# Optimization experiments

Measured on AMD Instinct MI355X. Metric: run time of the kernel, lower is better.

The kernel has to match this reference:

```python
import jax, jax.numpy as jnp
import numpy as np

B, N, DIN, DH, DOUT = 4096, 16, 256, 256, 256  # batch rows, num_variables, per-var dims


def _ln(x, g, b, eps=1e-5):
    m = jnp.mean(x, axis=-1, keepdims=True)
    v = jnp.var(x, axis=-1, keepdims=True)
    return (x - m) * jax.lax.rsqrt(v + eps) * g + b


def setup_inputs() -> dict:
    key = jax.random.key(0)
    ks = jax.random.split(key, 10)
    s = 0.02
    f32 = jnp.float32
    return {
        "x": jax.random.normal(ks[0], (B, N, DIN), f32),
        # per-variable GRN params, stacked along variable axis (batched GEMMs)
        "vW2": s * jax.random.normal(ks[1], (N, DIN, DH), f32),
        "vb2": jnp.zeros((N, DH), f32),
        "vW1": s * jax.random.normal(ks[2], (N, DH, DOUT), f32),
        "vb1": jnp.zeros((N, DOUT), f32),
        "vW4": s * jax.random.normal(ks[3], (N, DOUT, DOUT), f32),
        "vb4": jnp.zeros((N, DOUT), f32),
        "vW5": s * jax.random.normal(ks[4], (N, DOUT, DOUT), f32),
        "vb5": jnp.zeros((N, DOUT), f32),
        "vlng": jnp.ones((N, DOUT), f32),
        "vlnb": jnp.zeros((N, DOUT), f32),
        # concat GRN params (operate on flattened n*in features)
        "cW2": s * jax.random.normal(ks[5], (N * DIN, N * DH), f32),
        "cb2": jnp.zeros((N * DH,), f32),
        "cW1": s * jax.random.normal(ks[6], (N * DH, N * DOUT), f32),
        "cb1": jnp.zeros((N * DOUT,), f32),
        "cW4": s * jax.random.normal(ks[7], (N * DOUT, N * DOUT), f32),
        "cb4": jnp.zeros((N * DOUT,), f32),
        "cW5": s * jax.random.normal(ks[8], (N * DOUT, N * DOUT), f32),
        "cb5": jnp.zeros((N * DOUT,), f32),
        "clng": jnp.ones((N * DOUT,), f32),
        "clnb": jnp.zeros((N * DOUT,), f32),
    }


def reference(x, vW2, vb2, vW1, vb1, vW4, vb4, vW5, vb5, vlng, vlnb,
              cW2, cb2, cW1, cb1, cW4, cb4, cW5, cb5, clng, clnb):
    b = x.shape[0]
    flat = x.reshape(b, N * DIN)                       # torch.cat(inputs) over feature dim
    # ---- concat GRN: ELU dense -> dense -> GLU -> residual layernorm ----
    h = jax.nn.elu(flat @ cW2 + cb2)                   # [b, N*DH]
    e1 = h @ cW1 + cb1                                 # [b, N*DOUT]
    g = jax.nn.sigmoid(e1 @ cW4 + cb4) * (e1 @ cW5 + cb5)
    c = _ln(flat + g, clng, clnb)                      # [b, N*DOUT] (in==out, identity skip)
    # ---- softmax selection weights over the variable axis ----
    w = jax.nn.softmax(c.reshape(b, N, DOUT), axis=1)  # [b, N, DOUT]
    # ---- per-variable GRNs as batched GEMMs over the variable axis ----
    hv = jax.nn.elu(jnp.einsum('bni,nih->bnh', x, vW2) + vb2)
    e1v = jnp.einsum('bnh,nho->bno', hv, vW1) + vb1
    gv = (jax.nn.sigmoid(jnp.einsum('bno,nop->bnp', e1v, vW4) + vb4)
          * (jnp.einsum('bno,nop->bnp', e1v, vW5) + vb5))
    yv = _ln(x + gv, vlng, vlnb)                       # [b, N, DOUT]
    # ---- weighted combine (v^T @ x in the original) ----
    return jnp.sum(w * yv, axis=1)                     # [b, DOUT]
```

## Files before the change

### kernel.cpp

```cpp
#include <hip/hip_runtime.h>
#include <hip/hip_bf16.h>
#include <math.h>

typedef __hip_bfloat16 bf16;
typedef __attribute__((ext_vector_type(8))) short short8;
typedef __attribute__((ext_vector_type(4))) float f32x4;

#define DEV __device__ __forceinline__

DEV void gload_lds16(const bf16* g, bf16* l) {
    __builtin_amdgcn_global_load_lds(
        (__attribute__((address_space(1))) void*)(g),
        (__attribute__((address_space(3))) void*)(l), 16, 0, 0);
}

template<int ACT, bool DUAL>
__global__ __launch_bounds__(256, 2)
void gemm_k(const bf16* __restrict__ A, int lda, long aBatch,
            const bf16* __restrict__ B1p, const bf16* __restrict__ B2p,
            int ldb, long bBatch,
            const float* __restrict__ bias1p, const float* __restrict__ bias2p,
            long biasBatch,
            bf16* __restrict__ C, int ldc, long cBatch, int K)
{
    const int bz = blockIdx.z;
    A   += (long)bz * aBatch;
    const bf16* B1 = B1p + (long)bz * bBatch;
    const float* bias1 = bias1p + (long)bz * biasBatch;
    C   += (long)bz * cBatch;
    const bf16* B2 = nullptr;
    const float* bias2 = nullptr;
    if constexpr (DUAL) {
        B2 = B2p + (long)bz * bBatch;
        bias2 = bias2p + (long)bz * biasBatch;
    }

    const int rowBase = blockIdx.y * 128;
    const int colBase = blockIdx.x * 128;

    __shared__ bf16 As[128 * 32];
    __shared__ bf16 Bs[128 * 32];
    __shared__ bf16 Bs2[DUAL ? 128 * 32 : 8];

    const int tid  = threadIdx.x;
    const int wid  = tid >> 6;
    const int lane = tid & 63;
    const int wr = wid >> 1, wc = wid & 1;
    const int lr = lane & 15, lg = lane >> 4;

    f32x4 acc[4][4] = {};
    f32x4 acc2[4][4] = {};

    const int e0 = wid * 512 + lane * 8;
    const int sr = e0 >> 5;
    const int sc = e0 & 31;

    const bf16* a0 = A  + (long)(rowBase + sr)      * lda + sc;
    const bf16* a1 = A  + (long)(rowBase + sr + 64) * lda + sc;
    const bf16* b0 = B1 + (long)(colBase + sr)      * ldb + sc;
    const bf16* b1 = B1 + (long)(colBase + sr + 64) * ldb + sc;
    const bf16* d0 = nullptr; const bf16* d1 = nullptr;
    if constexpr (DUAL) {
        d0 = B2 + (long)(colBase + sr)      * ldb + sc;
        d1 = B2 + (long)(colBase + sr + 64) * ldb + sc;
    }

    bf16* AsW = As + wid * 512;
    bf16* BsW = Bs + wid * 512;
    bf16* Bs2W = nullptr;
    if constexpr (DUAL) Bs2W = Bs2 + wid * 512;

    for (int k0 = 0; k0 < K; k0 += 32) {
        gload_lds16(a0 + k0, AsW);
        gload_lds16(a1 + k0, AsW + 2048);
        gload_lds16(b0 + k0, BsW);
        gload_lds16(b1 + k0, BsW + 2048);
        if constexpr (DUAL) {
            gload_lds16(d0 + k0, Bs2W);
            gload_lds16(d1 + k0, Bs2W + 2048);
        }
        __syncthreads();

        short8 a[4], bb[4], b2[4];
        #pragma unroll
        for (int m = 0; m < 4; m++)
            a[m] = *(const short8*)(As + (wr * 64 + m * 16 + lr) * 32 + lg * 8);
        #pragma unroll
        for (int n = 0; n < 4; n++)
            bb[n] = *(const short8*)(Bs + (wc * 64 + n * 16 + lr) * 32 + lg * 8);
        if constexpr (DUAL) {
            #pragma unroll
            for (int n = 0; n < 4; n++)
                b2[n] = *(const short8*)(Bs2 + (wc * 64 + n * 16 + lr) * 32 + lg * 8);
        }

        #pragma unroll
        for (int m = 0; m < 4; m++) {
            #pragma unroll
            for (int n = 0; n < 4; n++) {
                acc[m][n] = __builtin_amdgcn_mfma_f32_16x16x32_bf16(a[m], bb[n], acc[m][n], 0, 0, 0);
                if constexpr (DUAL)
                    acc2[m][n] = __builtin_amdgcn_mfma_f32_16x16x32_bf16(a[m], b2[n], acc2[m][n], 0, 0, 0);
            }
        }
        __syncthreads();
    }

    #pragma unroll
    for (int m = 0; m < 4; m++) {
        const int row = rowBase + wr * 64 + m * 16 + lg * 4;
        #pragma unroll
        for (int n = 0; n < 4; n++) {
            const int col = colBase + wc * 64 + n * 16 + lr;
            const float bv1 = bias1[col];
            float bv2 = 0.f;
            if constexpr (DUAL) bv2 = bias2[col];
            #pragma unroll
            for (int i = 0; i < 4; i++) {
                float v = acc[m][n][i] + bv1;
                if constexpr (ACT == 1) v = v > 0.f ? v : expm1f(v);
                if constexpr (DUAL) {
                    float v2 = acc2[m][n][i] + bv2;
                    v = v2 / (1.f + expf(-v));
                }
                C[(long)(row + i) * ldc + col] = __float2bfloat16(v);
            }
        }
    }
}

__global__ __launch_bounds__(256)
void cvt_k(const float* __restrict__ in, bf16* __restrict__ out)
{
    const long i = ((long)blockIdx.x * 256 + threadIdx.x) * 8;
    float4 u = *(const float4*)(in + i);
    float4 v = *(const float4*)(in + i + 4);
    bf16 t[8];
    t[0] = __float2bfloat16(u.x); t[1] = __float2bfloat16(u.y);
    t[2] = __float2bfloat16(u.z); t[3] = __float2bfloat16(u.w);
    t[4] = __float2bfloat16(v.x); t[5] = __float2bfloat16(v.y);
    t[6] = __float2bfloat16(v.z); t[7] = __float2bfloat16(v.w);
    *(short8*)(out + i) = *(short8*)t;
}

struct TPtrs { const float* s[4]; bf16* d[4]; };

__global__ __launch_bounds__(256)
void transpose_cvt_k(TPtrs p, int R, int nsub)
{
    const int z = blockIdx.z;
    const int widx = z / nsub, sub = z - widx * nsub;
    const float* __restrict__ in = p.s[widx] + (long)sub * R * R;
    bf16* __restrict__ outp = p.d[widx] + (long)sub * R * R;

    __shared__ float tile[32][33];
    const int c0 = blockIdx.x * 32, r0 = blockIdx.y * 32;
    const int tx = threadIdx.x & 31, ty = threadIdx.x >> 5;
    #pragma unroll
    for (int i = 0; i < 4; i++)
        tile[ty + i * 8][tx] = in[(long)(r0 + ty + i * 8) * R + c0 + tx];
    __syncthreads();
    #pragma unroll
    for (int i = 0; i < 4; i++)
        outp[(long)(c0 + ty + i * 8) * R + r0 + tx] = __float2bfloat16(tile[tx][ty + i * 8]);
}

DEV float2 block_reduce2_bcast(float a, float b, float* lds)
{
    const int lane = threadIdx.x & 63, wid = threadIdx.x >> 6;
    #pragma unroll
    for (int off = 32; off > 0; off >>= 1) {
        a += __shfl_down(a, off, 64);
        b += __shfl_down(b, off, 64);
    }
    __syncthreads();
    if (lane == 0) { lds[wid] = a; lds[wid + 4] = b; }
    __syncthreads();
    float2 r;
    r.x = lds[0] + lds[1] + lds[2] + lds[3];
    r.y = lds[4] + lds[5] + lds[6] + lds[7];
    return r;
}

__global__ __launch_bounds__(256)
void ln_softmax_k(const float* __restrict__ x, const bf16* __restrict__ g,
                  const float* __restrict__ gamma, const float* __restrict__ beta,
                  bf16* __restrict__ w)
{
    const int b = blockIdx.x, d = threadIdx.x;
    const long base = (long)b * 4096;
    __shared__ float red[8];

    float s[16];
    float sum = 0.f, sumsq = 0.f;
    #pragma unroll
    for (int n = 0; n < 16; n++) {
        float v = x[base + n * 256 + d] + __bfloat162float(g[base + n * 256 + d]);
        s[n] = v; sum += v; sumsq += v * v;
    }
    float2 t = block_reduce2_bcast(sum, sumsq, red);
    const float mean = t.x * (1.f / 4096.f);
    const float var  = t.y * (1.f / 4096.f) - mean * mean;
    const float rstd = rsqrtf(var + 1e-5f);

    float mx = -1e30f;
    #pragma unroll
    for (int n = 0; n < 16; n++) {
        float c = (s[n] - mean) * rstd * gamma[n * 256 + d] + beta[n * 256 + d];
        s[n] = c; mx = fmaxf(mx, c);
    }
    float denom = 0.f;
    #pragma unroll
    for (int n = 0; n < 16; n++) { float e = expf(s[n] - mx); s[n] = e; denom += e; }
    const float rden = 1.f / denom;
    #pragma unroll
    for (int n = 0; n < 16; n++)
        w[base + n * 256 + d] = __float2bfloat16(s[n] * rden);
}

__global__ __launch_bounds__(256)
void combine_k(const float* __restrict__ x, const bf16* __restrict__ gv,
               const bf16* __restrict__ w,
               const float* __restrict__ vlng, const float* __restrict__ vlnb,
               float* __restrict__ out)
{
    const int b = blockIdx.x, d = threadIdx.x;
    const long base = (long)b * 4096;
    __shared__ float red[8];
    float acc = 0.f;
    for (int n = 0; n < 16; n++) {
        float v = x[base + n * 256 + d] + __bfloat162float(gv[base + n * 256 + d]);
        float2 t = block_reduce2_bcast(v, v * v, red);
        const float mean = t.x * (1.f / 256.f);
        const float var  = t.y * (1.f / 256.f) - mean * mean;
        const float yv = (v - mean) * rsqrtf(var + 1e-5f) * vlng[n * 256 + d] + vlnb[n * 256 + d];
        acc += __bfloat162float(w[base + n * 256 + d]) * yv;
    }
    out[(long)b * 256 + d] = acc;
}

extern "C" void kernel_launch(void* const* d_in, const int* in_sizes, int n_in,
                              void* d_out, int out_size, void* d_ws, size_t ws_size,
                              hipStream_t stream)
{
    const float* x    = (const float*)d_in[0];
    const float* vW2  = (const float*)d_in[1];
    const float* vb2  = (const float*)d_in[2];
    const float* vW1  = (const float*)d_in[3];
    const float* vb1  = (const float*)d_in[4];
    const float* vW4  = (const float*)d_in[5];
    const float* vb4  = (const float*)d_in[6];
    const float* vW5  = (const float*)d_in[7];
    const float* vb5  = (const float*)d_in[8];
    const float* vlng = (const float*)d_in[9];
    const float* vlnb = (const float*)d_in[10];
    const float* cW2  = (const float*)d_in[11];
    const float* cb2  = (const float*)d_in[12];
    const float* cW1  = (const float*)d_in[13];
    const float* cb1  = (const float*)d_in[14];
    const float* cW4  = (const float*)d_in[15];
    const float* cb4  = (const float*)d_in[16];
    const float* cW5  = (const float*)d_in[17];
    const float* cb5  = (const float*)d_in[18];
    const float* clng = (const float*)d_in[19];
    const float* clnb = (const float*)d_in[20];
    float* out = (float*)d_out;
    (void)n_in; (void)out_size; (void)ws_size;

    const int NB = in_sizes[0] / 4096;
    const long XF = (long)NB * 4096;

    char* ws = (char*)d_ws;
    size_t off = 0;
    auto alloc = [&](size_t bytes) {
        char* p = ws + off;
        off += (bytes + 255) & ~(size_t)255;
        return p;
    };
    bf16* xb   = (bf16*)alloc(XF * 2);
    bf16* cW2t = (bf16*)alloc(4096L * 4096 * 2);
    bf16* cW1t = (bf16*)alloc(4096L * 4096 * 2);
    bf16* cW4t = (bf16*)alloc(4096L * 4096 * 2);
    bf16* cW5t = (bf16*)alloc(4096L * 4096 * 2);
    bf16* vW2t = (bf16*)alloc(16L * 256 * 256 * 2);
    bf16* vW1t = (bf16*)alloc(16L * 256 * 256 * 2);
    bf16* vW4t = (bf16*)alloc(16L * 256 * 256 * 2);
    bf16* vW5t = (bf16*)alloc(16L * 256 * 256 * 2);
    bf16* bufA = (bf16*)alloc(XF * 2);
    bf16* bufB = (bf16*)alloc(XF * 2);
    bf16* bufW = (bf16*)alloc(XF * 2);

    const int MB = NB / 128;

    cvt_k<<<dim3((unsigned)(XF / 2048)), 256, 0, stream>>>(x, xb);

    TPtrs pb;
    pb.s[0] = cW2; pb.s[1] = cW1; pb.s[2] = cW4; pb.s[3] = cW5;
    pb.d[0] = cW2t; pb.d[1] = cW1t; pb.d[2] = cW4t; pb.d[3] = cW5t;
    transpose_cvt_k<<<dim3(128, 128, 4), 256, 0, stream>>>(pb, 4096, 1);

    TPtrs pv;
    pv.s[0] = vW2; pv.s[1] = vW1; pv.s[2] = vW4; pv.s[3] = vW5;
    pv.d[0] = vW2t; pv.d[1] = vW1t; pv.d[2] = vW4t; pv.d[3] = vW5t;
    transpose_cvt_k<<<dim3(8, 8, 64), 256, 0, stream>>>(pv, 256, 16);

    gemm_k<1, false><<<dim3(32, MB, 1), 256, 0, stream>>>(
        xb, 4096, 0, cW2t, nullptr, 4096, 0, cb2, nullptr, 0, bufA, 4096, 0, 4096);
    gemm_k<0, false><<<dim3(32, MB, 1), 256, 0, stream>>>(
        bufA, 4096, 0, cW1t, nullptr, 4096, 0, cb1, nullptr, 0, bufB, 4096, 0, 4096);
    gemm_k<0, true><<<dim3(32, MB, 1), 256, 0, stream>>>(
        bufB, 4096, 0, cW4t, cW5t, 4096, 0, cb4, cb5, 0, bufA, 4096, 0, 4096);
    ln_softmax_k<<<dim3(NB), 256, 0, stream>>>(x, bufA, clng, clnb, bufW);

    gemm_k<1, false><<<dim3(2, MB, 16), 256, 0, stream>>>(
        xb, 4096, 256, vW2t, nullptr, 256, 65536, vb2, nullptr, 256, bufB, 4096, 256, 256);
    gemm_k<0, false><<<dim3(2, MB, 16), 256, 0, stream>>>(
        bufB, 4096, 256, vW1t, nullptr, 256, 65536, vb1, nullptr, 256, bufA, 4096, 256, 256);
    gemm_k<0, true><<<dim3(2, MB, 16), 256, 0, stream>>>(
        bufA, 4096, 256, vW4t, vW5t, 256, 65536, vb4, vb5, 256, bufB, 4096, 256, 256);

    combine_k<<<dim3(NB), 256, 0, stream>>>(x, bufB, bufW, vlng, vlnb, out);
}
```

Before: 1.119 ms.

## Replace GEMM with 256x256 double-buffered pipelined kernel and split GLU GEMMs

Replaces the 128x128 single-buffered GEMM with a 512-thread 256x256 tile kernel. It uses 128KB of dynamic LDS double buffering, swizzled LDS layout, explicit vmcnt waits, quadrant-interleaved MFMA scheduling with setprio, and XCD-aware block remapping. The dual GLU GEMM is split into two single-output GEMMs, and the sigmoid gating moves into the LN/softmax and combine kernels. Dead transposed-weight buffers are reused as scratch for the extra outputs. The aim is better operand reuse and load/compute overlap, at the cost of extra intermediate traffic, fewer blocks per launch (only 16 per batched small GEMM), and more LDS pressure.

```diff
diff --git a/kernel.cpp b/kernel.cpp
--- a/kernel.cpp
+++ b/kernel.cpp
@@ -1,6 +1,7 @@
 #include <hip/hip_runtime.h>
 #include <hip/hip_bf16.h>
 #include <math.h>
+#include <type_traits>
 
 typedef __hip_bfloat16 bf16;
 typedef __attribute__((ext_vector_type(8))) short short8;
@@ -8,125 +9,164 @@
 
 #define DEV __device__ __forceinline__
 
+template<int V> using IC = std::integral_constant<int, V>;
+
 DEV void gload_lds16(const bf16* g, bf16* l) {
     __builtin_amdgcn_global_load_lds(
-        (__attribute__((address_space(1))) void*)(g),
+        (const __attribute__((address_space(1))) void*)(g),
         (__attribute__((address_space(3))) void*)(l), 16, 0, 0);
 }
 
-template<int ACT, bool DUAL>
-__global__ __launch_bounds__(256, 2)
-void gemm_k(const bf16* __restrict__ A, int lda, long aBatch,
-            const bf16* __restrict__ B1p, const bf16* __restrict__ B2p,
-            int ldb, long bBatch,
-            const float* __restrict__ bias1p, const float* __restrict__ bias2p,
-            long biasBatch,
-            bf16* __restrict__ C, int ldc, long cBatch, int K)
-{
+#define VMW(n) do { asm volatile("s_waitcnt vmcnt(" #n ")" ::: "memory"); \
+                    __builtin_amdgcn_sched_barrier(0); } while (0)
+
+template<int ACT>
+__global__ __launch_bounds__(512, 2)
+void gemm256_k(const bf16* __restrict__ Am, int lda, long aBatch,
+               const bf16* __restrict__ Bm, int ldb, long bBatch,
+               const float* __restrict__ biasp, long biasBatch,
+               bf16* __restrict__ Cm, int ldc, long cBatch, int K)
+{
+    extern __shared__ char lds[];
     const int bz = blockIdx.z;
-    A   += (long)bz * aBatch;
-    const bf16* B1 = B1p + (long)bz * bBatch;
-    const float* bias1 = bias1p + (long)bz * biasBatch;
-    C   += (long)bz * cBatch;
-    const bf16* B2 = nullptr;
-    const float* bias2 = nullptr;
-    if constexpr (DUAL) {
-        B2 = B2p + (long)bz * bBatch;
-        bias2 = bias2p + (long)bz * biasBatch;
-    }
-
-    const int rowBase = blockIdx.y * 128;
-    const int colBase = blockIdx.x * 128;
-
-    __shared__ bf16 As[128 * 32];
-    __shared__ bf16 Bs[128 * 32];
-    __shared__ bf16 Bs2[DUAL ? 128 * 32 : 8];
-
-    const int tid  = threadIdx.x;
-    const int wid  = tid >> 6;
-    const int lane = tid & 63;
-    const int wr = wid >> 1, wc = wid & 1;
+    const bf16* A = Am + (long)bz * aBatch;
+    const bf16* B = Bm + (long)bz * bBatch;
+    const float* bias = biasp + (long)bz * biasBatch;
+    bf16* C = Cm + (long)bz * cBatch;
+
+    const int nwg = gridDim.x * gridDim.y;
+    int flat = blockIdx.y * gridDim.x + blockIdx.x;
+    if ((nwg & 7) == 0 && nwg >= 8) flat = (flat & 7) * (nwg >> 3) + (flat >> 3);
+    const int bx = flat % gridDim.x, by = flat / gridDim.x;
+    const int rowBase = by * 256, colBase = bx * 256;
+
+    const int tid = threadIdx.x;
+    const int wid = tid >> 6, lane = tid & 63;
+    const int wr = wid >> 2, wc = wid & 3;
     const int lr = lane & 15, lg = lane >> 4;
 
-    f32x4 acc[4][4] = {};
-    f32x4 acc2[4][4] = {};
-
-    const int e0 = wid * 512 + lane * 8;
-    const int sr = e0 >> 5;
-    const int sc = e0 & 31;
-
-    const bf16* a0 = A  + (long)(rowBase + sr)      * lda + sc;
-    const bf16* a1 = A  + (long)(rowBase + sr + 64) * lda + sc;
-    const bf16* b0 = B1 + (long)(colBase + sr)      * ldb + sc;
-    const bf16* b1 = B1 + (long)(colBase + sr + 64) * ldb + sc;
-    const bf16* d0 = nullptr; const bf16* d1 = nullptr;
-    if constexpr (DUAL) {
-        d0 = B2 + (long)(colBase + sr)      * ldb + sc;
-        d1 = B2 + (long)(colBase + sr + 64) * ldb + sc;
-    }
-
-    bf16* AsW = As + wid * 512;
-    bf16* BsW = Bs + wid * 512;
-    bf16* Bs2W = nullptr;
-    if constexpr (DUAL) Bs2W = Bs2 + wid * 512;
-
-    for (int k0 = 0; k0 < K; k0 += 32) {
-        gload_lds16(a0 + k0, AsW);
-        gload_lds16(a1 + k0, AsW + 2048);
-        gload_lds16(b0 + k0, BsW);
-        gload_lds16(b1 + k0, BsW + 2048);
-        if constexpr (DUAL) {
-            gload_lds16(d0 + k0, Bs2W);
-            gload_lds16(d1 + k0, Bs2W + 2048);
-        }
-        __syncthreads();
-
-        short8 a[4], bb[4], b2[4];
+    const int r     = (tid >> 2) & 15;
+    const int cbyte = (tid & 3) * 16;
+    const int c0    = ((r & 8) ? (cbyte ^ 32) : cbyte) >> 1;
+    const int srow  = (wid >> 1) * 16 + r;
+    const int scol  = (wid & 1) * 32 + c0;
+
+    const bf16* Ap = A + (long)(rowBase + srow) * lda + scol;
+    const bf16* Bp = B + (long)(colBase + srow) * ldb + scol;
+
+    const int cb  = (lr & 8) ? ((lg * 16) ^ 32) : (lg * 16);
+    const int aRd = wr * 8192 + lr * 64 + cb;
+    const int bRd = wc * 4096 + lr * 64 + cb;
+
+    f32x4  acc[2][2][4][2] = {};
+    short8 aF[2][4][2];
+    short8 bF[2][2][2];
+
+    const int T = K >> 6;
+
+    auto stageA = [&](int tt, int h) {
+        bf16* d = (bf16*)(lds + (tt & 1) * 32768 + h * 16384 + wid * 1024);
+        const bf16* s = Ap + tt * 64 + (long)h * 128 * lda;
+        gload_lds16(s, d);
+        gload_lds16(s + (long)64 * lda, (bf16*)((char*)d + 8192));
+    };
+    auto stageB = [&](int tt, int h) {
+        bf16* d = (bf16*)(lds + 65536 + (tt & 1) * 32768 + h * 16384 + wid * 1024);
+        const bf16* s = Bp + tt * 64 + (long)h * 128 * ldb;
+        gload_lds16(s, d);
+        gload_lds16(s + (long)64 * ldb, (bf16*)((char*)d + 8192));
+    };
+    auto readA = [&](int tt, auto qmc) {
+        constexpr int qm = decltype(qmc)::value;
+        const char* base = lds + (tt & 1) * 32768 + qm * 16384 + aRd;
         #pragma unroll
-        for (int m = 0; m < 4; m++)
-            a[m] = *(const short8*)(As + (wr * 64 + m * 16 + lr) * 32 + lg * 8);
+        for (int mi = 0; mi < 4; mi++)
+            #pragma unroll
+            for (int ks = 0; ks < 2; ks++)
+                aF[qm][mi][ks] = *(const short8*)(base + mi * 2048 + ks * 1024);
+    };
+    auto readB = [&](int tt, auto qnc) {
+        constexpr int qn = decltype(qnc)::value;
+        const char* base = lds + 65536 + (tt & 1) * 32768 + qn * 16384 + bRd;
         #pragma unroll
-        for (int n = 0; n < 4; n++)
-            bb[n] = *(const short8*)(Bs + (wc * 64 + n * 16 + lr) * 32 + lg * 8);
-        if constexpr (DUAL) {
+        for (int ni = 0; ni < 2; ni++)
             #pragma unroll
-            for (int n = 0; n < 4; n++)
-                b2[n] = *(const short8*)(Bs2 + (wc * 64 + n * 16 + lr) * 32 + lg * 8);
-        }
-
+            for (int ks = 0; ks < 2; ks++)
+                bF[qn][ni][ks] = *(const short8*)(base + ni * 2048 + ks * 1024);
+    };
+    auto mma = [&](auto qmc, auto qnc) {
+        constexpr int qm = decltype(qmc)::value;
+        constexpr int qn = decltype(qnc)::value;
+        __builtin_amdgcn_s_setprio(1);
         #pragma unroll
-        for (int m = 0; m < 4; m++) {
+        for (int mi = 0; mi < 4; mi++)
+          #pragma unroll
+          for (int ni = 0; ni < 2; ni++)
             #pragma unroll
-            for (int n = 0; n < 4; n++) {
-                acc[m][n] = __builtin_amdgcn_mfma_f32_16x16x32_bf16(a[m], bb[n], acc[m][n], 0, 0, 0);
-                if constexpr (DUAL)
-                    acc2[m][n] = __builtin_amdgcn_mfma_f32_16x16x32_bf16(a[m], b2[n], acc2[m][n], 0, 0, 0);
-            }
-        }
-        __syncthreads();
-    }
-
-    #pragma unroll
-    for (int m = 0; m < 4; m++) {
-        const int row = rowBase + wr * 64 + m * 16 + lg * 4;
+            for (int ks = 0; ks < 2; ks++)
+              acc[qm][qn][mi][ni] = __builtin_amdgcn_mfma_f32_16x16x32_bf16(
+                  aF[qm][mi][ks], bF[qn][ni][ks], acc[qm][qn][mi][ni], 0, 0, 0);
+        __builtin_amdgcn_s_setprio(0);
+    };
+    auto bar = [&]() {
+        __builtin_amdgcn_sched_barrier(0);
+        __builtin_amdgcn_s_barrier();
+        __builtin_amdgcn_sched_barrier(0);
+    };
+
+    stageA(0, 0); stageB(0, 0); stageA(0, 1); stageB(0, 1);
+    if (T > 1) stageA(1, 0);
+    VMW(6);
+    bar();
+    readA(0, IC<0>{}); readB(0, IC<0>{});
+
+    for (int t = 0; t < T; t++) {
+        const bool last  = (t == T - 1);
+        const bool last2 = (t == T - 2);
+        if (!last) stageB(t + 1, 0);
+        if (!last) { VMW(6); } else { VMW(2); }
+        bar();
+        readA(t, IC<1>{});
+        mma(IC<0>{}, IC<0>{});
+        bar();
+        if (!last) stageA(t + 1, 1);
+        if (!last) { VMW(6); } else { VMW(0); }
+        bar();
+        readB(t, IC<1>{});
+        mma(IC<1>{}, IC<0>{});
+        bar();
+        if (!last) stageB(t + 1, 1);
+        bar();
+        mma(IC<1>{}, IC<1>{});
+        bar();
+        if (t + 2 < T) stageA(t + 2, 0);
+        if (!last) { if (last2) { VMW(4); } else { VMW(6); } }
+        bar();
+        mma(IC<0>{}, IC<1>{});
+        if (!last) { readA(t + 1, IC<0>{}); readB(t + 1, IC<0>{}); }
+        bar();
+    }
+
+    const long ldcL = ldc;
+    #pragma unroll
+    for (int qm = 0; qm < 2; qm++)
+      #pragma unroll
+      for (int mi = 0; mi < 4; mi++) {
+        const int row0 = rowBase + qm * 128 + wr * 64 + mi * 16 + lg * 4;
         #pragma unroll
-        for (int n = 0; n < 4; n++) {
-            const int col = colBase + wc * 64 + n * 16 + lr;
-            const float bv1 = bias1[col];
-            float bv2 = 0.f;
-            if constexpr (DUAL) bv2 = bias2[col];
+        for (int qn = 0; qn < 2; qn++)
+          #pragma unroll
+          for (int ni = 0; ni < 2; ni++) {
+            const int col = colBase + qn * 128 + wc * 32 + ni * 16 + lr;
+            const float bv = bias[col];
             #pragma unroll
             for (int i = 0; i < 4; i++) {
-                float v = acc[m][n][i] + bv1;
-                if constexpr (ACT == 1) v = v > 0.f ? v : expm1f(v);
-                if constexpr (DUAL) {
-                    float v2 = acc2[m][n][i] + bv2;
-                    v = v2 / (1.f + expf(-v));
-                }
-                C[(long)(row + i) * ldc + col] = __float2bfloat16(v);
+                float v = acc[qm][qn][mi][ni][i] + bv;
+                if (ACT == 1) v = v > 0.f ? v : expm1f(v);
+                C[(long)(row0 + i) * ldcL + col] = __float2bfloat16(v);
             }
-        }
-    }
+          }
+      }
 }
 
 __global__ __launch_bounds__(256)
@@ -165,7 +205,7 @@
         outp[(long)(c0 + ty + i * 8) * R + r0 + tx] = __float2bfloat16(tile[tx][ty + i * 8]);
 }
 
-DEV float2 block_reduce2_bcast(float a, float b, float* lds)
+DEV float2 block_reduce2_bcast(float a, float b, float* ldsr)
 {
     const int lane = threadIdx.x & 63, wid = threadIdx.x >> 6;
     #pragma unroll
@@ -174,16 +214,17 @@
         b += __shfl_down(b, off, 64);
     }
     __syncthreads();
-    if (lane == 0) { lds[wid] = a; lds[wid + 4] = b; }
+    if (lane == 0) { ldsr[wid] = a; ldsr[wid + 4] = b; }
     __syncthreads();
-    float2 r;
-    r.x = lds[0] + lds[1] + lds[2] + lds[3];
-    r.y = lds[4] + lds[5] + lds[6] + lds[7];
-    return r;
+    float2 rr;
+    rr.x = ldsr[0] + ldsr[1] + ldsr[2] + ldsr[3];
+    rr.y = ldsr[4] + ldsr[5] + ldsr[6] + ldsr[7];
+    return rr;
 }
 
 __global__ __launch_bounds__(256)
-void ln_softmax_k(const float* __restrict__ x, const bf16* __restrict__ g,
+void ln_softmax_k(const float* __restrict__ x,
+                  const bf16* __restrict__ e4, const bf16* __restrict__ e5,
                   const float* __restrict__ gamma, const float* __restrict__ beta,
                   bf16* __restrict__ w)
 {
@@ -195,7 +236,10 @@
     float sum = 0.f, sumsq = 0.f;
     #pragma unroll
     for (int n = 0; n < 16; n++) {
-        float v = x[base + n * 256 + d] + __bfloat162float(g[base + n * 256 + d]);
+        const long idx = base + n * 256 + d;
+        float g4 = __bfloat162float(e4[idx]);
+        float g5 = __bfloat162float(e5[idx]);
+        float v = x[idx] + g5 / (1.f + expf(-g4));
         s[n] = v; sum += v; sumsq += v * v;
     }
     float2 t = block_reduce2_bcast(sum, sumsq, red);
@@ -219,7 +263,8 @@
 }
 
 __global__ __launch_bounds__(256)
-void combine_k(const float* __restrict__ x, const bf16* __restrict__ gv,
+void combine_k(const float* __restrict__ x,
+               const bf16* __restrict__ e4v, const bf16* __restrict__ e5v,
                const bf16* __restrict__ w,
                const float* __restrict__ vlng, const float* __restrict__ vlnb,
                float* __restrict__ out)
@@ -229,12 +274,15 @@
     __shared__ float red[8];
     float acc = 0.f;
     for (int n = 0; n < 16; n++) {
-        float v = x[base + n * 256 + d] + __bfloat162float(gv[base + n * 256 + d]);
+        const long idx = base + n * 256 + d;
+        float g4 = __bfloat162float(e4v[idx]);
+        float g5 = __bfloat162float(e5v[idx]);
+        float v = x[idx] + g5 / (1.f + expf(-g4));
         float2 t = block_reduce2_bcast(v, v * v, red);
         const float mean = t.x * (1.f / 256.f);
         const float var  = t.y * (1.f / 256.f) - mean * mean;
         const float yv = (v - mean) * rsqrtf(var + 1e-5f) * vlng[n * 256 + d] + vlnb[n * 256 + d];
-        acc += __bfloat162float(w[base + n * 256 + d]) * yv;
+        acc += __bfloat162float(w[idx]) * yv;
     }
     out[(long)b * 256 + d] = acc;
 }
@@ -289,8 +337,15 @@
     bf16* bufA = (bf16*)alloc(XF * 2);
     bf16* bufB = (bf16*)alloc(XF * 2);
     bf16* bufW = (bf16*)alloc(XF * 2);
-
-    const int MB = NB / 128;
+    bf16* bufC = cW1t;
+    bf16* bufD = cW2t;
+
+    hipFuncSetAttribute(reinterpret_cast<const void*>(gemm256_k<0>),
+                        hipFuncAttributeMaxDynamicSharedMemorySize, 131072);
+    hipFuncSetAttribute(reinterpret_cast<const void*>(gemm256_k<1>),
+                        hipFuncAttributeMaxDynamicSharedMemorySize, 131072);
+
+    const int MB = NB / 256;
 
     cvt_k<<<dim3((unsigned)(XF / 2048)), 256, 0, stream>>>(x, xb);
 
@@ -304,20 +359,24 @@
     pv.d[0] = vW2t; pv.d[1] = vW1t; pv.d[2] = vW4t; pv.d[3] = vW5t;
     transpose_cvt_k<<<dim3(8, 8, 64), 256, 0, stream>>>(pv, 256, 16);
 
-    gemm_k<1, false><<<dim3(32, MB, 1), 256, 0, stream>>>(
-        xb, 4096, 0, cW2t, nullptr, 4096, 0, cb2, nullptr, 0, bufA, 4096, 0, 4096);
-    gemm_k<0, false><<<dim3(32, MB, 1), 256, 0, stream>>>(
-        bufA, 4096, 0, cW1t, nullptr, 4096, 0, cb1, nullptr, 0, bufB, 4096, 0, 4096);
-    gemm_k<0, true><<<dim3(32, MB, 1), 256, 0, stream>>>(
-        bufB, 4096, 0, cW4t, cW5t, 4096, 0, cb4, cb5, 0, bufA, 4096, 0, 4096);
-    ln_softmax_k<<<dim3(NB), 256, 0, stream>>>(x, bufA, clng, clnb, bufW);
-
-    gemm_k<1, false><<<dim3(2, MB, 16), 256, 0, stream>>>(
-        xb, 4096, 256, vW2t, nullptr, 256, 65536, vb2, nullptr, 256, bufB, 4096, 256, 256);
-    gemm_k<0, false><<<dim3(2, MB, 16), 256, 0, stream>>>(
-        bufB, 4096, 256, vW1t, nullptr, 256, 65536, vb1, nullptr, 256, bufA, 4096, 256, 256);
-    gemm_k<0, true><<<dim3(2, MB, 16), 256, 0, stream>>>(
-        bufA, 4096, 256, vW4t, vW5t, 256, 65536, vb4, vb5, 256, bufB, 4096, 256, 256);
-
-    combine_k<<<dim3(NB), 256, 0, stream>>>(x, bufB, bufW, vlng, vlnb, out);
-}
+    gemm256_k<1><<<dim3(16, MB, 1), 512, 131072, stream>>>(
+        xb, 4096, 0, cW2t, 4096, 0, cb2, 0, bufA, 4096, 0, 4096);
+    gemm256_k<0><<<dim3(16, MB, 1), 512, 131072, stream>>>(
+        bufA, 4096, 0, cW1t, 4096, 0, cb1, 0, bufB, 4096, 0, 4096);
+    gemm256_k<0><<<dim3(16, MB, 1), 512, 131072, stream>>>(
+        bufB, 4096, 0, cW4t, 4096, 0, cb4, 0, bufC, 4096, 0, 4096);
+    gemm256_k<0><<<dim3(16, MB, 1), 512, 131072, stream>>>(
+        bufB, 4096, 0, cW5t, 4096, 0, cb5, 0, bufD, 4096, 0, 4096);
+    ln_softmax_k<<<dim3(NB), 256, 0, stream>>>(x, bufC, bufD, clng, clnb, bufW);
+
+    gemm256_k<1><<<dim3(1, MB, 16), 512, 131072, stream>>>(
+        xb, 4096, 256, vW2t, 256, 65536, vb2, 256, bufA, 4096, 256, 256);
+    gemm256_k<0><<<dim3(1, MB, 16), 512, 131072, stream>>>(
+        bufA, 4096, 256, vW1t, 256, 65536, vb1, 256, bufB, 4096, 256, 256);
+    gemm256_k<0><<<dim3(1, MB, 16), 512, 131072, stream>>>(
+        bufB, 4096, 256, vW4t, 256, 65536, vb4, 256, bufC, 4096, 256, 256);
+    gemm256_k<0><<<dim3(1, MB, 16), 512, 131072, stream>>>(
+        bufB, 4096, 256, vW5t, 256, 65536, vb5, 256, bufD, 4096, 256, 256);
+
+    combine_k<<<dim3(NB), 256, 0, stream>>>(x, bufC, bufD, bufW, vlng, vlnb, out);
+}
```

Measured after the change: 1.069 ms. 1.05x faster.
